# Kernel tuning notes

Measured on AMD Instinct MI355X. Metric: run time of the kernel, lower is better.

Reference implementation:

```python
import math
import jax, jax.numpy as jnp
import numpy as np

P = 4096          # number of MC particles
H = 256           # hidden_layer_width
LEN_TIME = 100    # int(T / dt)
DT = 0.1
SQRT_DT = math.sqrt(DT)


def setup_inputs() -> dict:
    key = jax.random.key(0)
    ks = jax.random.split(key, 14)
    def lin(k, fan_in, fan_out):
        s = 1.0 / math.sqrt(fan_in)
        return jax.random.uniform(k, (fan_in, fan_out), jnp.float32, -s, s)
    return {
        "W0": lin(ks[0], 8, H),   "b0": jnp.zeros((H,), jnp.float32),
        "W1": lin(ks[1], H, H),   "b1": jnp.zeros((H,), jnp.float32),
        "W2": lin(ks[2], H, H),   "b2": jnp.zeros((H,), jnp.float32),
        "W3": lin(ks[3], H, 5),   "b3": jnp.zeros((5,), jnp.float32),
        "obs_init": jax.random.uniform(ks[4], (P, 1, 2), jnp.float32, 0.1, 1.0),
        "feature_init": jax.random.uniform(ks[5], (P, 1, 6), jnp.float32),
        "tn_store": jax.random.uniform(ks[6], (LEN_TIME - 1,), jnp.float32),
        "x1_store": jax.random.uniform(ks[7], (LEN_TIME - 1,), jnp.float32),
        "x2_store": jax.random.uniform(ks[8], (LEN_TIME - 1,), jnp.float32),
        "path_seed": jax.random.normal(ks[9], (LEN_TIME, P, 2), jnp.float32),
    }


def reference(W0, b0, W1, b1, W2, b2, W3, b3,
              obs_init, feature_init, tn_store, x1_store, x2_store, path_seed):
    def cell(x):  # x: (P, 8) -> mu (P,2), chol (P,2,2)  [RNNCell.forward]
        h = jax.nn.relu(x @ W0 + b0)
        h = jax.nn.relu(h @ W1 + b1)
        h = jax.nn.relu(h @ W2 + b2)
        out = h @ W3 + b3                      # (P, 5)
        mu = out[:, :2]
        s11 = jax.nn.softplus(out[:, 2])
        s21 = out[:, 3]
        s22 = jax.nn.softplus(out[:, 4])
        zeros = jnp.zeros_like(s11)
        chol = jnp.stack([jnp.stack([s11, zeros], -1),
                          jnp.stack([s21, s22], -1)], -2)  # (P, 2, 2)
        return mu, chol

    def sample(state, mu, chol, seed):  # _path_sampler, Test=False
        out = state + DT * mu + SQRT_DT * jnp.einsum('pij,pj->pi', chol, seed)
        return jax.nn.softplus(out)     # (P, 2)

    # step 0
    inp0 = jnp.concatenate([obs_init[:, 0, :], feature_init[:, 0, :]], -1)  # (P, 8)
    mu0, chol0 = cell(inp0)
    out0 = sample(inp0[:, :2], mu0, chol0, path_seed[0])
    t0 = feature_init[0, 0, 0]  # inp[0,0,2] of the initial input

    def step(carry, xs):
        state, t = carry
        tn, x1, x2, seed = xs
        t_new = t + DT
        feat = jnp.stack([t_new, tn, x1, x2, x1, x2])        # (6,) tiled features
        inp = jnp.concatenate([state, jnp.broadcast_to(feat, (P, 6))], -1)  # (P, 8)
        mu, chol = cell(inp)
        out = sample(state, mu, chol, seed)
        return (out, t_new), (mu, chol, out)

    (_, _), (mus, chols, outs) = jax.lax.scan(
        step, (out0, t0), (tn_store, x1_store, x2_store, path_seed[1:]))

    # assemble stores: path (P, LEN_TIME+1, 2), mu (P*LEN_TIME, 2), sigma (P*LEN_TIME, 2, 2)
    path = jnp.concatenate([obs_init[:, 0, :][:, None, :],
                            out0[:, None, :],
                            jnp.moveaxis(outs, 0, 1)], 1)
    mu_store = jnp.concatenate([mu0[:, None, :], jnp.moveaxis(mus, 0, 1)], 1).reshape(-1, 2)
    sigma_store = jnp.concatenate([chol0[:, None], jnp.moveaxis(chols, 0, 1)], 1).reshape(-1, 2, 2)
    return path.transpose(0, 2, 1), mu_store, sigma_store
```

## Files before the change

### kernel.cpp

```cpp
#include <hip/hip_runtime.h>
#include <math.h>


#define PP 4096
#define HH 256
#define LT 100
#define PB 16
#define SH 264
#define NT 1024

typedef __attribute__((ext_vector_type(8))) short short8;
typedef __attribute__((ext_vector_type(4))) short short4v;
typedef __attribute__((ext_vector_type(4))) float float4v;

__device__ __forceinline__ float softplus_fast(float x) {
    const float e = __expf(-fabsf(x));
    return fmaxf(x, 0.0f) + __logf(1.0f + e);
}
__device__ __forceinline__ unsigned short f2bf(float f) {
    unsigned int u = __float_as_uint(f);
    u += 0x7fffu + ((u >> 16) & 1u);
    return (unsigned short)(u >> 16);
}
__device__ __forceinline__ float4 ldg4(const float* p) { return *(const float4*)p; }

__global__ void prep_cfeat(const float* __restrict__ W0, const float* __restrict__ b0,
                           const float* __restrict__ feature_init,
                           const float* __restrict__ tn_store,
                           const float* __restrict__ x1_store,
                           const float* __restrict__ x2_store,
                           float* __restrict__ cfeat) {
    const int t = blockIdx.x + 1;
    const int col = threadIdx.x;
    float tval = feature_init[0];
    for (int i = 0; i < t; ++i) tval += 0.1f;
    const float tn = tn_store[t - 1], x1 = x1_store[t - 1], x2 = x2_store[t - 1];
    const float w2c = W0[2 * 256 + col], w3c = W0[3 * 256 + col];
    const float w46 = W0[4 * 256 + col] + W0[6 * 256 + col];
    const float w57 = W0[5 * 256 + col] + W0[7 * 256 + col];
    cfeat[t * 256 + col] = b0[col] + tval * w2c + tn * w3c + x1 * w46 + x2 * w57;
}

__device__ __forceinline__ void mfma256_reg1(const short8 (&wf)[8], float bv,
                                             const unsigned short* __restrict__ hin,
                                             unsigned short* __restrict__ hout,
                                             int wv, int lane) {
    const int quad = lane >> 4, col = lane & 15;
    float4v acc = {bv, bv, bv, bv};
    const unsigned short* arow = hin + col * SH + quad * 8;
#pragma unroll
    for (int ks = 0; ks < 8; ++ks) {
        short8 a = *(const short8*)(arow + ks * 32);
        acc = __builtin_amdgcn_mfma_f32_16x16x32_bf16(a, wf[ks], acc, 0, 0, 0);
    }
#pragma unroll
    for (int r = 0; r < 4; ++r) {
        hout[(quad * 4 + r) * SH + wv * 16 + col] = f2bf(fmaxf(acc[r], 0.0f));
    }
}

__global__ __launch_bounds__(NT, 1)
void lv_kernel(const float* __restrict__ W0, const float* __restrict__ b0,
               const float* __restrict__ W1, const float* __restrict__ b1,
               const float* __restrict__ W2, const float* __restrict__ b2,
               const float* __restrict__ W3, const float* __restrict__ b3,
               const float* __restrict__ obs_init, const float* __restrict__ feature_init,
               const float* __restrict__ path_seed,
               const float* __restrict__ cfeat,
               float* __restrict__ out) {
    __shared__ unsigned short hA[PB * SH];
    __shared__ unsigned short hB[PB * SH];
    __shared__ unsigned short hC[PB * SH];
    __shared__ __align__(16) unsigned short w3l[4096];
    __shared__ __align__(16) float w0l[512];
    __shared__ float sc[16][5];
    __shared__ float st[PB][2];
    __shared__ __align__(16) float pbuf[PB * 202];
    __shared__ __align__(16) float mbuf[PB * 200];
    __shared__ __align__(16) float sbuf[PB * 400];

    const int tid = threadIdx.x;
    const int lane = tid & 63;
    const int wv = tid >> 6;
    const int quad = lane >> 4;
    const int col = lane & 15;
    const int pbase = blockIdx.x * PB;

    const float DTf = 0.1f;
    const float SQ = 0.31622776601683794f;

    short8 wf1[8], wf2[8];
    {
        const int colc = wv * 16 + col;
#pragma unroll
        for (int ks = 0; ks < 8; ++ks) {
#pragma unroll
            for (int j = 0; j < 8; ++j) {
                const int k = ks * 32 + quad * 8 + j;
                wf1[ks][j] = (short)f2bf(W1[k * 256 + colc]);
                wf2[ks][j] = (short)f2bf(W2[k * 256 + colc]);
            }
        }
    }
    for (int e = tid; e < 4096; e += NT) {
        const int j = e & 7, ln = (e >> 3) & 63, ks = e >> 9;
        const int k = ks * 32 + (ln >> 4) * 8 + j;
        const int n = ln & 15;
        w3l[e] = (n < 5) ? f2bf(W3[k * 5 + n]) : (unsigned short)0;
    }
    if (tid < 512) w0l[tid] = W0[tid];

    const float bv1 = b1[wv * 16 + col];
    const float bv2 = b2[wv * 16 + col];
    const float b3c = (col < 5) ? b3[col] : 0.0f;

    if (tid < PB) {
        const int p = tid, gp = pbase + p;
        pbuf[p * 202 + 0] = obs_init[gp * 2 + 0];
        pbuf[p * 202 + 101] = obs_init[gp * 2 + 1];
    }

    {
        const int gp = pbase + wv;
        float xk[8];
        xk[0] = obs_init[gp * 2 + 0];
        xk[1] = obs_init[gp * 2 + 1];
#pragma unroll
        for (int f = 0; f < 6; ++f) xk[2 + f] = feature_init[gp * 6 + f];
        const int c0 = lane * 4;
        const float4 bv = ldg4(b0 + c0);
        float a0 = bv.x, a1 = bv.y, a2 = bv.z, a3 = bv.w;
#pragma unroll
        for (int k = 0; k < 8; ++k) {
            const float4 w = ldg4(W0 + k * HH + c0);
            a0 = fmaf(xk[k], w.x, a0); a1 = fmaf(xk[k], w.y, a1);
            a2 = fmaf(xk[k], w.z, a2); a3 = fmaf(xk[k], w.w, a3);
        }
        short4v o;
        o[0] = (short)f2bf(fmaxf(a0, 0.0f));
        o[1] = (short)f2bf(fmaxf(a1, 0.0f));
        o[2] = (short)f2bf(fmaxf(a2, 0.0f));
        o[3] = (short)f2bf(fmaxf(a3, 0.0f));
        *(short4v*)&hA[wv * SH + c0] = o;
    }
    float4 cf = ldg4(cfeat + 256 + lane * 4);

    for (int t = 0; t < LT; ++t) {
        float e0 = 0.0f, e1 = 0.0f;
        if (tid < PB) {
            const int gp = pbase + tid;
            e0 = path_seed[(size_t)t * PP * 2 + gp * 2 + 0];
            e1 = path_seed[(size_t)t * PP * 2 + gp * 2 + 1];
        }

        if (t > 0) {
            const float s0 = st[wv][0];
            const float s1 = st[wv][1];
            const int c0 = lane * 4;
            const float4 wa = *(const float4*)&w0l[c0];
            const float4 wb = *(const float4*)&w0l[256 + c0];
            short4v o;
            o[0] = (short)f2bf(fmaxf(fmaf(s0, wa.x, fmaf(s1, wb.x, cf.x)), 0.0f));
            o[1] = (short)f2bf(fmaxf(fmaf(s0, wa.y, fmaf(s1, wb.y, cf.y)), 0.0f));
            o[2] = (short)f2bf(fmaxf(fmaf(s0, wa.z, fmaf(s1, wb.z, cf.z)), 0.0f));
            o[3] = (short)f2bf(fmaxf(fmaf(s0, wa.w, fmaf(s1, wb.w, cf.w)), 0.0f));
            *(short4v*)&hA[wv * SH + c0] = o;
        }
        {
            const int ti = (t + 1 < LT) ? (t + 1) : (LT - 1);
            cf = ldg4(cfeat + ti * 256 + lane * 4);
        }
        __syncthreads();

        mfma256_reg1(wf1, bv1, hA, hB, wv, lane);
        __syncthreads();
        mfma256_reg1(wf2, bv2, hB, hC, wv, lane);
        __syncthreads();

        if (wv == 0) {
            float4v accA = {b3c, b3c, b3c, b3c};
            float4v accB = {0.0f, 0.0f, 0.0f, 0.0f};
            const unsigned short* arow = hC + col * SH + quad * 8;
#pragma unroll
            for (int ks = 0; ks < 4; ++ks) {
                short8 a0 = *(const short8*)(arow + ks * 32);
                short8 a1 = *(const short8*)(arow + (ks + 4) * 32);
                short8 b0f = *(const short8*)(w3l + (ks * 64 + lane) * 8);
                short8 b1f = *(const short8*)(w3l + ((ks + 4) * 64 + lane) * 8);
                accA = __builtin_amdgcn_mfma_f32_16x16x32_bf16(a0, b0f, accA, 0, 0, 0);
                accB = __builtin_amdgcn_mfma_f32_16x16x32_bf16(a1, b1f, accB, 0, 0, 0);
            }
            if (col < 5) {
#pragma unroll
                for (int r = 0; r < 4; ++r) sc[quad * 4 + r][col] = accA[r] + accB[r];
            }
            if (lane < 16) {
                const int p = lane;
                const float mu0 = sc[p][0];
                const float mu1 = sc[p][1];
                const float s11 = softplus_fast(sc[p][2]);
                const float s21 = sc[p][3];
                const float s22 = softplus_fast(sc[p][4]);
                const float ps0 = (t == 0) ? pbuf[p * 202 + 0] : st[p][0];
                const float ps1 = (t == 0) ? pbuf[p * 202 + 101] : st[p][1];
                const float n0 = softplus_fast(ps0 + DTf * mu0 + SQ * (s11 * e0));
                const float n1 = softplus_fast(ps1 + DTf * mu1 + SQ * (s21 * e0 + s22 * e1));
                st[p][0] = n0;
                st[p][1] = n1;
                pbuf[p * 202 + (t + 1)] = n0;
                pbuf[p * 202 + 101 + (t + 1)] = n1;
                mbuf[p * 200 + t * 2 + 0] = mu0;
                mbuf[p * 200 + t * 2 + 1] = mu1;
                sbuf[p * 400 + t * 4 + 0] = s11;
                sbuf[p * 400 + t * 4 + 1] = 0.0f;
                sbuf[p * 400 + t * 4 + 2] = s21;
                sbuf[p * 400 + t * 4 + 3] = s22;
            }
        }
        __syncthreads();
    }

    float* __restrict__ pdst = out + (size_t)pbase * 202;
    float* __restrict__ mdst = out + (size_t)PP * 202 + (size_t)pbase * 200;
    float* __restrict__ sdst = out + (size_t)PP * 202 + (size_t)PP * 200 + (size_t)pbase * 400;
    for (int i = tid; i < PB * 202 / 4; i += NT) ((float4*)pdst)[i] = ((const float4*)pbuf)[i];
    for (int i = tid; i < PB * 200 / 4; i += NT) ((float4*)mdst)[i] = ((const float4*)mbuf)[i];
    for (int i = tid; i < PB * 400 / 4; i += NT) ((float4*)sdst)[i] = ((const float4*)sbuf)[i];
}

extern "C" void kernel_launch(void* const* d_in, const int* in_sizes, int n_in,
                              void* d_out, int out_size, void* d_ws, size_t ws_size,
                              hipStream_t stream) {
    (void)in_sizes; (void)n_in; (void)out_size; (void)ws_size;
    float* cfeat = (float*)d_ws;
    prep_cfeat<<<LT - 1, 256, 0, stream>>>(
        (const float*)d_in[0],
        (const float*)d_in[1],
        (const float*)d_in[9],
        (const float*)d_in[10],
        (const float*)d_in[11],
        (const float*)d_in[12],
        cfeat);
    lv_kernel<<<PP / PB, NT, 0, stream>>>(
        (const float*)d_in[0],
        (const float*)d_in[1],
        (const float*)d_in[2],
        (const float*)d_in[3],
        (const float*)d_in[4],
        (const float*)d_in[5],
        (const float*)d_in[6],
        (const float*)d_in[7],
        (const float*)d_in[8],
        (const float*)d_in[9],
        (const float*)d_in[13],
        cfeat,
        (float*)d_out);
}
```

Measured before the change: 322.4 us.

## Halve block to 512 threads with two column tiles per wave, two blocks per CU

Each block now runs 8 waves instead of 16. Every wave computes two 16-column MFMA output tiles with register-resident W1/W2 fragments, sharing the A-operand load between them. The layer-0 and state-update work is remapped so each half-wave handles one particle with 8 columns per lane. Launch bounds now allow two blocks per CU, which is meant to cut per-block barrier cost and let another block fill the latency of this one's serial timestep chain. In exchange each thread holds twice as many weight registers (32 short8 per thread), which may cause spills or cap occupancy.

```diff
diff --git a/kernel.cpp b/kernel.cpp
--- a/kernel.cpp
+++ b/kernel.cpp
@@ -7,7 +7,7 @@
 #define LT 100
 #define PB 16
 #define SH 264
-#define NT 1024
+#define NT 512
 
 typedef __attribute__((ext_vector_type(8))) short short8;
 typedef __attribute__((ext_vector_type(4))) short short4v;
@@ -41,25 +41,28 @@
     cfeat[t * 256 + col] = b0[col] + tval * w2c + tn * w3c + x1 * w46 + x2 * w57;
 }
 
-__device__ __forceinline__ void mfma256_reg1(const short8 (&wf)[8], float bv,
+__device__ __forceinline__ void mfma256_reg2(const short8 (&wf)[2][8], float bv0, float bv1,
                                              const unsigned short* __restrict__ hin,
                                              unsigned short* __restrict__ hout,
                                              int wv, int lane) {
     const int quad = lane >> 4, col = lane & 15;
-    float4v acc = {bv, bv, bv, bv};
+    float4v acc0 = {bv0, bv0, bv0, bv0};
+    float4v acc1 = {bv1, bv1, bv1, bv1};
     const unsigned short* arow = hin + col * SH + quad * 8;
 #pragma unroll
     for (int ks = 0; ks < 8; ++ks) {
         short8 a = *(const short8*)(arow + ks * 32);
-        acc = __builtin_amdgcn_mfma_f32_16x16x32_bf16(a, wf[ks], acc, 0, 0, 0);
+        acc0 = __builtin_amdgcn_mfma_f32_16x16x32_bf16(a, wf[0][ks], acc0, 0, 0, 0);
+        acc1 = __builtin_amdgcn_mfma_f32_16x16x32_bf16(a, wf[1][ks], acc1, 0, 0, 0);
     }
 #pragma unroll
     for (int r = 0; r < 4; ++r) {
-        hout[(quad * 4 + r) * SH + wv * 16 + col] = f2bf(fmaxf(acc[r], 0.0f));
-    }
-}
-
-__global__ __launch_bounds__(NT, 1)
+        hout[(quad * 4 + r) * SH + wv * 32 + col]      = f2bf(fmaxf(acc0[r], 0.0f));
+        hout[(quad * 4 + r) * SH + wv * 32 + 16 + col] = f2bf(fmaxf(acc1[r], 0.0f));
+    }
+}
+
+__global__ __launch_bounds__(NT, 2)
 void lv_kernel(const float* __restrict__ W0, const float* __restrict__ b0,
                const float* __restrict__ W1, const float* __restrict__ b1,
                const float* __restrict__ W2, const float* __restrict__ b2,
@@ -84,21 +87,26 @@
     const int wv = tid >> 6;
     const int quad = lane >> 4;
     const int col = lane & 15;
+    const int hl = lane & 31;
+    const int lp = 2 * wv + (lane >> 5);
     const int pbase = blockIdx.x * PB;
 
     const float DTf = 0.1f;
     const float SQ = 0.31622776601683794f;
 
-    short8 wf1[8], wf2[8];
+    short8 wf1[2][8], wf2[2][8];
     {
-        const int colc = wv * 16 + col;
-#pragma unroll
-        for (int ks = 0; ks < 8; ++ks) {
-#pragma unroll
-            for (int j = 0; j < 8; ++j) {
-                const int k = ks * 32 + quad * 8 + j;
-                wf1[ks][j] = (short)f2bf(W1[k * 256 + colc]);
-                wf2[ks][j] = (short)f2bf(W2[k * 256 + colc]);
+#pragma unroll
+        for (int g = 0; g < 2; ++g) {
+            const int colc = wv * 32 + g * 16 + col;
+#pragma unroll
+            for (int ks = 0; ks < 8; ++ks) {
+#pragma unroll
+                for (int j = 0; j < 8; ++j) {
+                    const int k = ks * 32 + quad * 8 + j;
+                    wf1[g][ks][j] = (short)f2bf(W1[k * 256 + colc]);
+                    wf2[g][ks][j] = (short)f2bf(W2[k * 256 + colc]);
+                }
             }
         }
     }
@@ -108,10 +116,12 @@
         const int n = ln & 15;
         w3l[e] = (n < 5) ? f2bf(W3[k * 5 + n]) : (unsigned short)0;
     }
-    if (tid < 512) w0l[tid] = W0[tid];
-
-    const float bv1 = b1[wv * 16 + col];
-    const float bv2 = b2[wv * 16 + col];
+    w0l[tid] = W0[tid];
+
+    const float bv1a = b1[wv * 32 + col];
+    const float bv1b = b1[wv * 32 + 16 + col];
+    const float bv2a = b2[wv * 32 + col];
+    const float bv2b = b2[wv * 32 + 16 + col];
     const float b3c = (col < 5) ? b3[col] : 0.0f;
 
     if (tid < PB) {
@@ -121,29 +131,36 @@
     }
 
     {
-        const int gp = pbase + wv;
+        const int gp = pbase + lp;
         float xk[8];
         xk[0] = obs_init[gp * 2 + 0];
         xk[1] = obs_init[gp * 2 + 1];
 #pragma unroll
         for (int f = 0; f < 6; ++f) xk[2 + f] = feature_init[gp * 6 + f];
-        const int c0 = lane * 4;
-        const float4 bv = ldg4(b0 + c0);
-        float a0 = bv.x, a1 = bv.y, a2 = bv.z, a3 = bv.w;
+        const int c0 = hl * 8;
+        float a[8];
+        {
+            const float4 ba = ldg4(b0 + c0);
+            const float4 bb = ldg4(b0 + c0 + 4);
+            a[0] = ba.x; a[1] = ba.y; a[2] = ba.z; a[3] = ba.w;
+            a[4] = bb.x; a[5] = bb.y; a[6] = bb.z; a[7] = bb.w;
+        }
 #pragma unroll
         for (int k = 0; k < 8; ++k) {
-            const float4 w = ldg4(W0 + k * HH + c0);
-            a0 = fmaf(xk[k], w.x, a0); a1 = fmaf(xk[k], w.y, a1);
-            a2 = fmaf(xk[k], w.z, a2); a3 = fmaf(xk[k], w.w, a3);
-        }
-        short4v o;
-        o[0] = (short)f2bf(fmaxf(a0, 0.0f));
-        o[1] = (short)f2bf(fmaxf(a1, 0.0f));
-        o[2] = (short)f2bf(fmaxf(a2, 0.0f));
-        o[3] = (short)f2bf(fmaxf(a3, 0.0f));
-        *(short4v*)&hA[wv * SH + c0] = o;
-    }
-    float4 cf = ldg4(cfeat + 256 + lane * 4);
+            const float4 wa = ldg4(W0 + k * HH + c0);
+            const float4 wb = ldg4(W0 + k * HH + c0 + 4);
+            a[0] = fmaf(xk[k], wa.x, a[0]); a[1] = fmaf(xk[k], wa.y, a[1]);
+            a[2] = fmaf(xk[k], wa.z, a[2]); a[3] = fmaf(xk[k], wa.w, a[3]);
+            a[4] = fmaf(xk[k], wb.x, a[4]); a[5] = fmaf(xk[k], wb.y, a[5]);
+            a[6] = fmaf(xk[k], wb.z, a[6]); a[7] = fmaf(xk[k], wb.w, a[7]);
+        }
+        short8 o;
+#pragma unroll
+        for (int j = 0; j < 8; ++j) o[j] = (short)f2bf(fmaxf(a[j], 0.0f));
+        *(short8*)&hA[lp * SH + c0] = o;
+    }
+    float4 cf0 = ldg4(cfeat + 256 + hl * 8);
+    float4 cf1 = ldg4(cfeat + 256 + hl * 8 + 4);
 
     for (int t = 0; t < LT; ++t) {
         float e0 = 0.0f, e1 = 0.0f;
@@ -154,27 +171,34 @@
         }
 
         if (t > 0) {
-            const float s0 = st[wv][0];
-            const float s1 = st[wv][1];
-            const int c0 = lane * 4;
-            const float4 wa = *(const float4*)&w0l[c0];
-            const float4 wb = *(const float4*)&w0l[256 + c0];
-            short4v o;
-            o[0] = (short)f2bf(fmaxf(fmaf(s0, wa.x, fmaf(s1, wb.x, cf.x)), 0.0f));
-            o[1] = (short)f2bf(fmaxf(fmaf(s0, wa.y, fmaf(s1, wb.y, cf.y)), 0.0f));
-            o[2] = (short)f2bf(fmaxf(fmaf(s0, wa.z, fmaf(s1, wb.z, cf.z)), 0.0f));
-            o[3] = (short)f2bf(fmaxf(fmaf(s0, wa.w, fmaf(s1, wb.w, cf.w)), 0.0f));
-            *(short4v*)&hA[wv * SH + c0] = o;
+            const float s0 = st[lp][0];
+            const float s1 = st[lp][1];
+            const int c0 = hl * 8;
+            const float4 wa0 = *(const float4*)&w0l[c0];
+            const float4 wa1 = *(const float4*)&w0l[c0 + 4];
+            const float4 wb0 = *(const float4*)&w0l[256 + c0];
+            const float4 wb1 = *(const float4*)&w0l[256 + c0 + 4];
+            short8 o;
+            o[0] = (short)f2bf(fmaxf(fmaf(s0, wa0.x, fmaf(s1, wb0.x, cf0.x)), 0.0f));
+            o[1] = (short)f2bf(fmaxf(fmaf(s0, wa0.y, fmaf(s1, wb0.y, cf0.y)), 0.0f));
+            o[2] = (short)f2bf(fmaxf(fmaf(s0, wa0.z, fmaf(s1, wb0.z, cf0.z)), 0.0f));
+            o[3] = (short)f2bf(fmaxf(fmaf(s0, wa0.w, fmaf(s1, wb0.w, cf0.w)), 0.0f));
+            o[4] = (short)f2bf(fmaxf(fmaf(s0, wa1.x, fmaf(s1, wb1.x, cf1.x)), 0.0f));
+            o[5] = (short)f2bf(fmaxf(fmaf(s0, wa1.y, fmaf(s1, wb1.y, cf1.y)), 0.0f));
+            o[6] = (short)f2bf(fmaxf(fmaf(s0, wa1.z, fmaf(s1, wb1.z, cf1.z)), 0.0f));
+            o[7] = (short)f2bf(fmaxf(fmaf(s0, wa1.w, fmaf(s1, wb1.w, cf1.w)), 0.0f));
+            *(short8*)&hA[lp * SH + c0] = o;
         }
         {
             const int ti = (t + 1 < LT) ? (t + 1) : (LT - 1);
-            cf = ldg4(cfeat + ti * 256 + lane * 4);
-        }
-        __syncthreads();
-
-        mfma256_reg1(wf1, bv1, hA, hB, wv, lane);
-        __syncthreads();
-        mfma256_reg1(wf2, bv2, hB, hC, wv, lane);
+            cf0 = ldg4(cfeat + ti * 256 + hl * 8);
+            cf1 = ldg4(cfeat + ti * 256 + hl * 8 + 4);
+        }
+        __syncthreads();
+
+        mfma256_reg2(wf1, bv1a, bv1b, hA, hB, wv, lane);
+        __syncthreads();
+        mfma256_reg2(wf2, bv2a, bv2b, hB, hC, wv, lane);
         __syncthreads();
 
         if (wv == 0) {
```

After: 286.8 us. 11.0% less time.

## Shrink block to 4 waves, each computing 64 output columns with A-fragment reuse

Applied to the files above, without the earlier changes.

Reduces the block from 1024 to 256 threads; each wave now holds weight fragments for four 16-column groups and issues four MFMAs per loaded A fragment. The first-layer and feature-update code is remapped so each thread handles 16 columns of one particle. This is meant to cut barrier cost and LDS reads per step, at the price of much higher register pressure and longer serial MFMA chains per wave.

```diff
diff --git a/kernel.cpp b/kernel.cpp
--- a/kernel.cpp
+++ b/kernel.cpp
@@ -7,7 +7,7 @@
 #define LT 100
 #define PB 16
 #define SH 264
-#define NT 1024
+#define NT 256
 
 typedef __attribute__((ext_vector_type(8))) short short8;
 typedef __attribute__((ext_vector_type(4))) short short4v;
@@ -41,21 +41,28 @@
     cfeat[t * 256 + col] = b0[col] + tval * w2c + tn * w3c + x1 * w46 + x2 * w57;
 }
 
-__device__ __forceinline__ void mfma256_reg1(const short8 (&wf)[8], float bv,
+__device__ __forceinline__ void mfma256_reg4(const short8 (&wf)[4][8], const float (&bv)[4],
                                              const unsigned short* __restrict__ hin,
                                              unsigned short* __restrict__ hout,
                                              int wv, int lane) {
     const int quad = lane >> 4, col = lane & 15;
-    float4v acc = {bv, bv, bv, bv};
+    float4v acc[4];
+#pragma unroll
+    for (int g = 0; g < 4; ++g) acc[g] = (float4v){bv[g], bv[g], bv[g], bv[g]};
     const unsigned short* arow = hin + col * SH + quad * 8;
 #pragma unroll
     for (int ks = 0; ks < 8; ++ks) {
         short8 a = *(const short8*)(arow + ks * 32);
-        acc = __builtin_amdgcn_mfma_f32_16x16x32_bf16(a, wf[ks], acc, 0, 0, 0);
-    }
-#pragma unroll
-    for (int r = 0; r < 4; ++r) {
-        hout[(quad * 4 + r) * SH + wv * 16 + col] = f2bf(fmaxf(acc[r], 0.0f));
+#pragma unroll
+        for (int g = 0; g < 4; ++g)
+            acc[g] = __builtin_amdgcn_mfma_f32_16x16x32_bf16(a, wf[g][ks], acc[g], 0, 0, 0);
+    }
+#pragma unroll
+    for (int g = 0; g < 4; ++g) {
+#pragma unroll
+        for (int r = 0; r < 4; ++r) {
+            hout[(quad * 4 + r) * SH + wv * 64 + g * 16 + col] = f2bf(fmaxf(acc[g][r], 0.0f));
+        }
     }
 }
 
@@ -84,21 +91,26 @@
     const int wv = tid >> 6;
     const int quad = lane >> 4;
     const int col = lane & 15;
+    const int lp = tid >> 4;
+    const int c0 = (tid & 15) * 16;
     const int pbase = blockIdx.x * PB;
 
     const float DTf = 0.1f;
     const float SQ = 0.31622776601683794f;
 
-    short8 wf1[8], wf2[8];
+    short8 wf1[4][8], wf2[4][8];
     {
-        const int colc = wv * 16 + col;
-#pragma unroll
-        for (int ks = 0; ks < 8; ++ks) {
-#pragma unroll
-            for (int j = 0; j < 8; ++j) {
-                const int k = ks * 32 + quad * 8 + j;
-                wf1[ks][j] = (short)f2bf(W1[k * 256 + colc]);
-                wf2[ks][j] = (short)f2bf(W2[k * 256 + colc]);
+#pragma unroll
+        for (int g = 0; g < 4; ++g) {
+            const int colc = wv * 64 + g * 16 + col;
+#pragma unroll
+            for (int ks = 0; ks < 8; ++ks) {
+#pragma unroll
+                for (int j = 0; j < 8; ++j) {
+                    const int k = ks * 32 + quad * 8 + j;
+                    wf1[g][ks][j] = (short)f2bf(W1[k * 256 + colc]);
+                    wf2[g][ks][j] = (short)f2bf(W2[k * 256 + colc]);
+                }
             }
         }
     }
@@ -108,10 +120,14 @@
         const int n = ln & 15;
         w3l[e] = (n < 5) ? f2bf(W3[k * 5 + n]) : (unsigned short)0;
     }
-    if (tid < 512) w0l[tid] = W0[tid];
-
-    const float bv1 = b1[wv * 16 + col];
-    const float bv2 = b2[wv * 16 + col];
+    for (int e = tid; e < 512; e += NT) w0l[e] = W0[e];
+
+    float bv1[4], bv2[4];
+#pragma unroll
+    for (int g = 0; g < 4; ++g) {
+        bv1[g] = b1[wv * 64 + g * 16 + col];
+        bv2[g] = b2[wv * 64 + g * 16 + col];
+    }
     const float b3c = (col < 5) ? b3[col] : 0.0f;
 
     if (tid < PB) {
@@ -121,29 +137,41 @@
     }
 
     {
-        const int gp = pbase + wv;
+        const int gp = pbase + lp;
         float xk[8];
         xk[0] = obs_init[gp * 2 + 0];
         xk[1] = obs_init[gp * 2 + 1];
 #pragma unroll
         for (int f = 0; f < 6; ++f) xk[2 + f] = feature_init[gp * 6 + f];
-        const int c0 = lane * 4;
-        const float4 bv = ldg4(b0 + c0);
-        float a0 = bv.x, a1 = bv.y, a2 = bv.z, a3 = bv.w;
+        float a[16];
+#pragma unroll
+        for (int i = 0; i < 4; ++i) {
+            const float4 bq = ldg4(b0 + c0 + 4 * i);
+            a[4 * i + 0] = bq.x; a[4 * i + 1] = bq.y; a[4 * i + 2] = bq.z; a[4 * i + 3] = bq.w;
+        }
 #pragma unroll
         for (int k = 0; k < 8; ++k) {
-            const float4 w = ldg4(W0 + k * HH + c0);
-            a0 = fmaf(xk[k], w.x, a0); a1 = fmaf(xk[k], w.y, a1);
-            a2 = fmaf(xk[k], w.z, a2); a3 = fmaf(xk[k], w.w, a3);
-        }
-        short4v o;
-        o[0] = (short)f2bf(fmaxf(a0, 0.0f));
-        o[1] = (short)f2bf(fmaxf(a1, 0.0f));
-        o[2] = (short)f2bf(fmaxf(a2, 0.0f));
-        o[3] = (short)f2bf(fmaxf(a3, 0.0f));
-        *(short4v*)&hA[wv * SH + c0] = o;
-    }
-    float4 cf = ldg4(cfeat + 256 + lane * 4);
+#pragma unroll
+            for (int i = 0; i < 4; ++i) {
+                const float4 w = ldg4(W0 + k * HH + c0 + 4 * i);
+                a[4 * i + 0] = fmaf(xk[k], w.x, a[4 * i + 0]);
+                a[4 * i + 1] = fmaf(xk[k], w.y, a[4 * i + 1]);
+                a[4 * i + 2] = fmaf(xk[k], w.z, a[4 * i + 2]);
+                a[4 * i + 3] = fmaf(xk[k], w.w, a[4 * i + 3]);
+            }
+        }
+        short8 o0, o1;
+#pragma unroll
+        for (int j = 0; j < 8; ++j) {
+            o0[j] = (short)f2bf(fmaxf(a[j], 0.0f));
+            o1[j] = (short)f2bf(fmaxf(a[8 + j], 0.0f));
+        }
+        *(short8*)&hA[lp * SH + c0] = o0;
+        *(short8*)&hA[lp * SH + c0 + 8] = o1;
+    }
+    float4 cf[4];
+#pragma unroll
+    for (int i = 0; i < 4; ++i) cf[i] = ldg4(cfeat + 256 + c0 + 4 * i);
 
     for (int t = 0; t < LT; ++t) {
         float e0 = 0.0f, e1 = 0.0f;
@@ -154,27 +182,39 @@
         }
 
         if (t > 0) {
-            const float s0 = st[wv][0];
-            const float s1 = st[wv][1];
-            const int c0 = lane * 4;
-            const float4 wa = *(const float4*)&w0l[c0];
-            const float4 wb = *(const float4*)&w0l[256 + c0];
-            short4v o;
-            o[0] = (short)f2bf(fmaxf(fmaf(s0, wa.x, fmaf(s1, wb.x, cf.x)), 0.0f));
-            o[1] = (short)f2bf(fmaxf(fmaf(s0, wa.y, fmaf(s1, wb.y, cf.y)), 0.0f));
-            o[2] = (short)f2bf(fmaxf(fmaf(s0, wa.z, fmaf(s1, wb.z, cf.z)), 0.0f));
-            o[3] = (short)f2bf(fmaxf(fmaf(s0, wa.w, fmaf(s1, wb.w, cf.w)), 0.0f));
-            *(short4v*)&hA[wv * SH + c0] = o;
+            const float s0 = st[lp][0];
+            const float s1 = st[lp][1];
+            short8 o0, o1;
+#pragma unroll
+            for (int i = 0; i < 4; ++i) {
+                const float4 wa = *(const float4*)&w0l[c0 + 4 * i];
+                const float4 wb = *(const float4*)&w0l[256 + c0 + 4 * i];
+                const int base = 4 * i;
+                const float v0 = fmaxf(fmaf(s0, wa.x, fmaf(s1, wb.x, cf[i].x)), 0.0f);
+                const float v1 = fmaxf(fmaf(s0, wa.y, fmaf(s1, wb.y, cf[i].y)), 0.0f);
+                const float v2 = fmaxf(fmaf(s0, wa.z, fmaf(s1, wb.z, cf[i].z)), 0.0f);
+                const float v3 = fmaxf(fmaf(s0, wa.w, fmaf(s1, wb.w, cf[i].w)), 0.0f);
+                if (i < 2) {
+                    o0[base + 0] = (short)f2bf(v0); o0[base + 1] = (short)f2bf(v1);
+                    o0[base + 2] = (short)f2bf(v2); o0[base + 3] = (short)f2bf(v3);
+                } else {
+                    o1[base - 8 + 0] = (short)f2bf(v0); o1[base - 8 + 1] = (short)f2bf(v1);
+                    o1[base - 8 + 2] = (short)f2bf(v2); o1[base - 8 + 3] = (short)f2bf(v3);
+                }
+            }
+            *(short8*)&hA[lp * SH + c0] = o0;
+            *(short8*)&hA[lp * SH + c0 + 8] = o1;
         }
         {
             const int ti = (t + 1 < LT) ? (t + 1) : (LT - 1);
-            cf = ldg4(cfeat + ti * 256 + lane * 4);
-        }
-        __syncthreads();
-
-        mfma256_reg1(wf1, bv1, hA, hB, wv, lane);
-        __syncthreads();
-        mfma256_reg1(wf2, bv2, hB, hC, wv, lane);
+#pragma unroll
+            for (int i = 0; i < 4; ++i) cf[i] = ldg4(cfeat + ti * 256 + c0 + 4 * i);
+        }
+        __syncthreads();
+
+        mfma256_reg4(wf1, bv1, hA, hB, wv, lane);
+        __syncthreads();
+        mfma256_reg4(wf2, bv2, hB, hC, wv, lane);
         __syncthreads();
 
         if (wv == 0) {
```

Result: slower. 426.2 us (+32.2%).
